# Kernel tuning notes

Hardware: AMD Instinct MI355X
Metric: run time of the kernel (lower is better)

## Reference

```python
import jax, jax.numpy as jnp
import numpy as np

B, HH, WW = 4, 112, 112
DIM, NH, WS, SHIFT = 384, 12, 7, 3
N = WS * WS
HD = DIM // NH
SCALE = HD ** -0.5
HID = DIM * 4
NW = (HH // WS) * (WW // WS)


def _ln(x, w, b):
    m = x.mean(-1, keepdims=True)
    v = ((x - m) ** 2).mean(-1, keepdims=True)
    return (x - m) / jnp.sqrt(v + 1e-5) * w + b


def _win_part(x):  # (B,H,W,C) -> (B*nW, N, C)
    x = x.reshape(B, HH // WS, WS, WW // WS, WS, DIM).transpose(0, 1, 3, 2, 4, 5)
    return x.reshape(-1, N, DIM)


def _win_rev(w):  # (B*nW, N, C) -> (B,H,W,C)
    x = w.reshape(B, HH // WS, WW // WS, WS, WS, DIM).transpose(0, 1, 3, 2, 4, 5)
    return x.reshape(B, HH, WW, DIM)


def _rel_index():
    c = np.arange(WS)
    coords = np.stack(np.meshgrid(c, c, indexing='ij')).reshape(2, -1)
    rel = (coords[:, :, None] - coords[:, None, :]).transpose(1, 2, 0).copy()
    rel[:, :, 0] += WS - 1
    rel[:, :, 1] += WS - 1
    rel[:, :, 0] *= 2 * WS - 1
    return rel.sum(-1)  # (N, N)


def _attn_mask():
    img = np.zeros((HH, WW))
    cnt = 0
    for hs in (slice(0, -WS), slice(-WS, -SHIFT), slice(-SHIFT, None)):
        for ws_ in (slice(0, -WS), slice(-WS, -SHIFT), slice(-SHIFT, None)):
            img[hs, ws_] = cnt
            cnt += 1
    mw = img.reshape(HH // WS, WS, WW // WS, WS).transpose(0, 2, 1, 3).reshape(-1, N)
    am = mw[:, None, :] - mw[:, :, None]
    return np.where(am != 0, -100.0, 0.0).astype(np.float32)  # (nW, N, N)


def setup_inputs():
    key = jax.random.key(0)
    ks = iter(jax.random.split(key, 32))
    rn = lambda shape, s=0.02: jax.random.normal(next(ks), shape, jnp.float32) * s
    return {
        'branch_1': jax.random.normal(next(ks), (B, HH * WW, DIM), jnp.float32),
        'branch_2': jax.random.normal(next(ks), (B, HH * WW, DIM), jnp.float32),
        'mask_matrix': jnp.asarray(_attn_mask()),
        'rpi': jnp.asarray(_rel_index(), jnp.int32),
        'n1w1': jnp.ones((DIM,)), 'n1b1': jnp.zeros((DIM,)),
        'n1w2': jnp.ones((DIM,)), 'n1b2': jnp.zeros((DIM,)),
        'qw1': rn((3 * DIM, DIM)), 'qb1': jnp.zeros((3 * DIM,)),
        'qw2': rn((3 * DIM, DIM)), 'qb2': jnp.zeros((3 * DIM,)),
        'rpb1': rn(((2 * WS - 1) ** 2, NH)), 'rpb2': rn(((2 * WS - 1) ** 2, NH)),
        'pw1': rn((DIM, DIM)), 'pb1': jnp.zeros((DIM,)),
        'pw2': rn((DIM, DIM)), 'pb2': jnp.zeros((DIM,)),
        'n2w1': jnp.ones((DIM,)), 'n2b1': jnp.zeros((DIM,)),
        'n2w2': jnp.ones((DIM,)), 'n2b2': jnp.zeros((DIM,)),
        'm1fc1w': rn((HID, DIM)), 'm1fc1b': jnp.zeros((HID,)),
        'm1fc2w': rn((DIM, HID)), 'm1fc2b': jnp.zeros((DIM,)),
        'm2fc1w': rn((HID, DIM)), 'm2fc1b': jnp.zeros((HID,)),
        'm2fc2w': rn((DIM, HID)), 'm2fc2b': jnp.zeros((DIM,)),
    }


def _cross_attn(x1, x2, mask, rpi, qw1, qb1, qw2, qb2, rpb1, rpb2, pw1, pb1, pw2, pb2):
    Bw = x1.shape[0]

    def qkv(x, w, b):
        t = (x @ w.T + b).reshape(Bw, N, 3, NH, HD).transpose(2, 0, 3, 1, 4)
        return t[0], t[1], t[2]

    q1, k1, v1 = qkv(x1, qw1, qb1)
    q2, k2, v2 = qkv(x2, qw2, qb2)
    a1 = (q2 * SCALE) @ jnp.swapaxes(k1, -2, -1)  # (Bw, NH, N, N)
    a2 = (q1 * SCALE) @ jnp.swapaxes(k2, -2, -1)
    b1 = rpb1[rpi].transpose(2, 0, 1)  # (NH, N, N)
    b2 = rpb2[rpi].transpose(2, 0, 1)
    a1 = a1 + b1[None]
    a2 = a2 + b2[None]
    nW = mask.shape[0]
    a1 = (a1.reshape(Bw // nW, nW, NH, N, N) + mask[None, :, None]).reshape(Bw, NH, N, N)
    a2 = (a2.reshape(Bw // nW, nW, NH, N, N) + mask[None, :, None]).reshape(Bw, NH, N, N)
    a1 = jax.nn.softmax(a1, axis=-1)
    a2 = jax.nn.softmax(a2, axis=-1)
    o1 = (a1 @ v1).transpose(0, 2, 1, 3).reshape(Bw, N, DIM) @ pw1.T + pb1
    o2 = (a2 @ v2).transpose(0, 2, 1, 3).reshape(Bw, N, DIM) @ pw2.T + pb2
    del o2
    return o1, o1  # faithful to original: it returns [branch_1, branch_1]


def _mlp(x, w1, b1, w2, b2):
    return jax.nn.gelu(x @ w1.T + b1, approximate=False) @ w2.T + b2


def reference(branch_1, branch_2, mask_matrix, rpi, n1w1, n1b1, n1w2, n1b2,
              qw1, qb1, qw2, qb2, rpb1, rpb2, pw1, pb1, pw2, pb2,
              n2w1, n2b1, n2w2, n2b2,
              m1fc1w, m1fc1b, m1fc2w, m1fc2b, m2fc1w, m2fc1b, m2fc2w, m2fc2b):
    s1, s2 = branch_1, branch_2
    x1 = _ln(branch_1, n1w1, n1b1).reshape(B, HH, WW, DIM)
    x2 = _ln(branch_2, n1w2, n1b2).reshape(B, HH, WW, DIM)
    # cyclic shift (shift_size > 0; H,W divisible by window_size so no padding)
    x1 = jnp.roll(x1, (-SHIFT, -SHIFT), (1, 2))
    x2 = jnp.roll(x2, (-SHIFT, -SHIFT), (1, 2))
    w1, w2 = _win_part(x1), _win_part(x2)
    o1, o2 = _cross_attn(w1, w2, mask_matrix, rpi, qw1, qb1, qw2, qb2,
                         rpb1, rpb2, pw1, pb1, pw2, pb2)
    y1 = jnp.roll(_win_rev(o1), (SHIFT, SHIFT), (1, 2)).reshape(B, HH * WW, DIM)
    y2 = jnp.roll(_win_rev(o2), (SHIFT, SHIFT), (1, 2)).reshape(B, HH * WW, DIM)
    b1 = s1 + y1
    b2 = s2 + y2
    out1 = b1 + _mlp(_ln(b1, n2w1, n2b1), m1fc1w, m1fc1b, m1fc2w, m1fc2b)
    out2 = b2 + _mlp(_ln(b2, n2w2, n2b2), m2fc1w, m2fc1b, m2fc2w, m2fc2b)
    return out1, out2
```

## Files before the change

### kernel.cpp

```cpp
#include <hip/hip_runtime.h>
#include <math.h>

#define DEV __device__ __forceinline__

typedef __attribute__((ext_vector_type(8))) unsigned short u16x8;
typedef __attribute__((ext_vector_type(8))) __bf16 bf16x8;
typedef __attribute__((ext_vector_type(4))) float f32x4;

static constexpr int TOK = 50176;
static constexpr int DIMC = 384;
static constexpr float QSCALE = 0.17677669529663687f;

DEV unsigned short f2bf(float f) {
  union { float f; unsigned u; } v; v.f = f;
  unsigned r = v.u + 0x7fffu + ((v.u >> 16) & 1u);
  return (unsigned short)(r >> 16);
}

DEV f32x4 mfma16(bf16x8 a, bf16x8 b, f32x4 c) {
  return __builtin_amdgcn_mfma_f32_16x16x32_bf16(a, b, c, 0, 0, 0);
}

DEV void gload_lds16(const void* g, void* lds) {
  __builtin_amdgcn_global_load_lds(
      (const __attribute__((address_space(1))) void*)g,
      (__attribute__((address_space(3))) void*)lds, 16, 0, 0);
}

__global__ __launch_bounds__(256) void w2bf_kern(const float* __restrict__ in,
                                                 unsigned short* __restrict__ out, int n) {
  int i = blockIdx.x * 256 + threadIdx.x;
  if (i < n) out[i] = f2bf(in[i]);
}

template<bool WINDOW>
__global__ __launch_bounds__(256) void ln_kern(const float* __restrict__ in,
                                               const float* __restrict__ gw,
                                               const float* __restrict__ gb,
                                               unsigned short* __restrict__ out) {
  const int row = blockIdx.x * 4 + (threadIdx.x >> 6);
  const int l = threadIdx.x & 63;
  int src = row;
  if (WINDOW) {
    const int wq = row / 49, nn = row - wq * 49;
    const int bb = wq >> 8, wi = wq & 255;
    int hh = (wi >> 4) * 7 + nn / 7 + 3;        if (hh >= 112) hh -= 112;
    int cc = (wi & 15) * 7 + (nn - (nn / 7) * 7) + 3; if (cc >= 112) cc -= 112;
    src = bb * 12544 + hh * 112 + cc;
  }
  const float* x = in + (size_t)src * DIMC;
  float v[6]; float s = 0.f, s2 = 0.f;
#pragma unroll
  for (int j = 0; j < 6; ++j) { float t = x[l + 64 * j]; v[j] = t; s += t; s2 += t * t; }
#pragma unroll
  for (int d = 1; d < 64; d <<= 1) { s += __shfl_xor(s, d); s2 += __shfl_xor(s2, d); }
  const float mean = s * (1.f / 384.f);
  const float var = s2 * (1.f / 384.f) - mean * mean;
  const float rs = rsqrtf(var + 1e-5f);
#pragma unroll
  for (int j = 0; j < 6; ++j) {
    int c = l + 64 * j;
    out[(size_t)row * DIMC + c] = f2bf((v[j] - mean) * rs * gw[c] + gb[c]);
  }
}

enum { E_BF16 = 0, E_BF16_SCALE = 1, E_SCATTER = 2, E_GELU = 3, E_RESOUT = 4 };

template<int EPI>
__global__ __launch_bounds__(256) void gemm_bt(
    const unsigned short* __restrict__ A, const unsigned short* __restrict__ W,
    const float* __restrict__ bias, int K, int N,
    unsigned short* __restrict__ outb,
    float* __restrict__ outf1, float* __restrict__ outf2,
    const float* __restrict__ res1, const float* __restrict__ res2) {
  __shared__ __align__(16) unsigned short sA[128 * 32];
  __shared__ __align__(16) unsigned short sB[128 * 32];
  const int t = threadIdx.x;
  const int wv = t >> 6, l = t & 63;
  const int wm = (wv >> 1) * 64, wn = (wv & 1) * 64;
  const int m0 = blockIdx.x * 128, n0 = blockIdx.y * 128;
  const int srow = t >> 2, scol = (t & 3) * 8;

  f32x4 acc[4][4];
  const f32x4 fzero = {0.f, 0.f, 0.f, 0.f};
#pragma unroll
  for (int i = 0; i < 4; ++i)
#pragma unroll
    for (int j = 0; j < 4; ++j) acc[i][j] = fzero;

  const unsigned short* gA = A + (size_t)(m0 + srow) * K + scol;
  const unsigned short* gB = W + (size_t)(n0 + srow) * K + scol;

  for (int kt = 0; kt < K; kt += 32) {
    __syncthreads();
#pragma unroll
    for (int it = 0; it < 2; ++it) {
      gload_lds16(gA + (size_t)it * 64 * K + kt, &sA[it * 2048 + wv * 512]);
      gload_lds16(gB + (size_t)it * 64 * K + kt, &sB[it * 2048 + wv * 512]);
    }
    __syncthreads();
    bf16x8 af[4], bff[4];
#pragma unroll
    for (int mt = 0; mt < 4; ++mt)
      af[mt] = *(const bf16x8*)&sA[(wm + mt * 16 + (l & 15)) * 32 + ((l >> 4) << 3)];
#pragma unroll
    for (int nt = 0; nt < 4; ++nt)
      bff[nt] = *(const bf16x8*)&sB[(wn + nt * 16 + (l & 15)) * 32 + ((l >> 4) << 3)];
#pragma unroll
    for (int mt = 0; mt < 4; ++mt)
#pragma unroll
      for (int nt = 0; nt < 4; ++nt) acc[mt][nt] = mfma16(af[mt], bff[nt], acc[mt][nt]);
  }

  const int g = l >> 4, col = l & 15;
#pragma unroll
  for (int mt = 0; mt < 4; ++mt) {
#pragma unroll
    for (int r = 0; r < 4; ++r) {
      const int m = m0 + wm + mt * 16 + g * 4 + r;
      size_t obase = 0;
      if constexpr (EPI == E_SCATTER) {
        int wq = m / 49, nn = m - wq * 49;
        int bb = wq >> 8, wi = wq & 255;
        int hh = (wi >> 4) * 7 + nn / 7 + 3;        if (hh >= 112) hh -= 112;
        int cc = (wi & 15) * 7 + (nn - (nn / 7) * 7) + 3; if (cc >= 112) cc -= 112;
        obase = ((size_t)bb * 12544 + hh * 112 + cc) * 384;
      }
#pragma unroll
      for (int nt = 0; nt < 4; ++nt) {
        const int j = n0 + wn + nt * 16 + col;
        float v = acc[mt][nt][r] + bias[j];
        if constexpr (EPI == E_BF16) {
          outb[(size_t)m * N + j] = f2bf(v);
        } else if constexpr (EPI == E_BF16_SCALE) {
          outb[(size_t)m * N + j] = f2bf(v * QSCALE);
        } else if constexpr (EPI == E_GELU) {
          outb[(size_t)m * N + j] = f2bf(0.5f * v * (1.f + erff(v * 0.70710678118654752f)));
        } else if constexpr (EPI == E_SCATTER) {
          outf1[obase + j] = res1[obase + j] + v;
          outf2[obase + j] = res2[obase + j] + v;
        } else {
          outf1[(size_t)m * N + j] = v + res1[(size_t)m * N + j];
        }
      }
    }
  }
}

__global__ __launch_bounds__(256) void attn_kern(
    const unsigned short* __restrict__ q2,
    const unsigned short* __restrict__ kv1,
    const int* __restrict__ rpi,
    const float* __restrict__ mask,
    const float* __restrict__ rpb,
    unsigned short* __restrict__ o) {
  const int w = blockIdx.x, h = blockIdx.y;
  __shared__ __align__(16) unsigned short sQ[64 * 32];
  __shared__ __align__(16) unsigned short sK[64 * 32];
  __shared__ __align__(16) unsigned short sVT[32 * 64];
  __shared__ __align__(16) unsigned short sP[64 * 64];
  const int t = threadIdx.x, wv = t >> 6, l = t & 63;
  const int r = t >> 2, c = (t & 3) * 8;
  const u16x8 z8 = {0, 0, 0, 0, 0, 0, 0, 0};
  if (r < 49) {
    *(u16x8*)&sQ[r * 32 + c] = *(const u16x8*)&q2[((size_t)w * 49 + r) * 384 + h * 32 + c];
    *(u16x8*)&sK[r * 32 + c] = *(const u16x8*)&kv1[((size_t)w * 49 + r) * 768 + h * 32 + c];
    u16x8 vv = *(const u16x8*)&kv1[((size_t)w * 49 + r) * 768 + 384 + h * 32 + c];
#pragma unroll
    for (int e = 0; e < 8; ++e) sVT[(c + e) * 64 + r] = vv[e];
  } else {
    *(u16x8*)&sQ[r * 32 + c] = z8;
    *(u16x8*)&sK[r * 32 + c] = z8;
#pragma unroll
    for (int e = 0; e < 8; ++e) sVT[(c + e) * 64 + r] = 0;
  }
  __syncthreads();

  const int g = l >> 4, col = l & 15;
  const f32x4 fzero = {0.f, 0.f, 0.f, 0.f};
  bf16x8 aq = *(const bf16x8*)&sQ[(wv * 16 + col) * 32 + g * 8];
  f32x4 s[4];
#pragma unroll
  for (int nt = 0; nt < 4; ++nt) {
    bf16x8 bk = *(const bf16x8*)&sK[(nt * 16 + col) * 32 + g * 8];
    s[nt] = mfma16(aq, bk, fzero);
  }

  const int wi = w & 255;
  float p[4][4];
#pragma unroll
  for (int rr = 0; rr < 4; ++rr) {
    const int i = wv * 16 + g * 4 + rr;
    float mx = -1e30f;
#pragma unroll
    for (int nt = 0; nt < 4; ++nt) {
      const int j = nt * 16 + col;
      float val = -1e9f;
      if (i < 49 && j < 49)
        val = s[nt][rr] + rpb[rpi[i * 49 + j] * 12 + h] + mask[((size_t)wi * 49 + i) * 49 + j];
      p[nt][rr] = val;
      mx = fmaxf(mx, val);
    }
#pragma unroll
    for (int d = 1; d < 16; d <<= 1) mx = fmaxf(mx, __shfl_xor(mx, d));
    float sm = 0.f;
#pragma unroll
    for (int nt = 0; nt < 4; ++nt) {
      const int j = nt * 16 + col;
      float e = (j < 49) ? __expf(p[nt][rr] - mx) : 0.f;
      p[nt][rr] = e; sm += e;
    }
#pragma unroll
    for (int d = 1; d < 16; d <<= 1) sm += __shfl_xor(sm, d);
    const float inv = 1.f / sm;
#pragma unroll
    for (int nt = 0; nt < 4; ++nt) p[nt][rr] *= inv;
  }
#pragma unroll
  for (int rr = 0; rr < 4; ++rr) {
    const int i = wv * 16 + g * 4 + rr;
#pragma unroll
    for (int nt = 0; nt < 4; ++nt) sP[i * 64 + nt * 16 + col] = f2bf(p[nt][rr]);
  }
  __syncthreads();

  f32x4 oa[2] = {fzero, fzero};
#pragma unroll
  for (int ks = 0; ks < 2; ++ks) {
    bf16x8 ap = *(const bf16x8*)&sP[(wv * 16 + col) * 64 + ks * 32 + g * 8];
#pragma unroll
    for (int n2 = 0; n2 < 2; ++n2) {
      bf16x8 bv = *(const bf16x8*)&sVT[(n2 * 16 + col) * 64 + ks * 32 + g * 8];
      oa[n2] = mfma16(ap, bv, oa[n2]);
    }
  }
#pragma unroll
  for (int rr = 0; rr < 4; ++rr) {
    const int i = wv * 16 + g * 4 + rr;
    if (i < 49) {
#pragma unroll
      for (int n2 = 0; n2 < 2; ++n2)
        o[((size_t)w * 49 + i) * 384 + h * 32 + n2 * 16 + col] = f2bf(oa[n2][rr]);
    }
  }
}

extern "C" void kernel_launch(void* const* d_in, const int* in_sizes, int n_in,
                              void* d_out, int out_size, void* d_ws, size_t ws_size,
                              hipStream_t stream) {
  (void)in_sizes; (void)n_in; (void)out_size; (void)ws_size;
  const float* s1   = (const float*)d_in[0];
  const float* s2   = (const float*)d_in[1];
  const float* mask = (const float*)d_in[2];
  const int*   rpi  = (const int*)d_in[3];
  const float* n1w1 = (const float*)d_in[4],  *n1b1 = (const float*)d_in[5];
  const float* n1w2 = (const float*)d_in[6],  *n1b2 = (const float*)d_in[7];
  const float* qw1  = (const float*)d_in[8],  *qb1  = (const float*)d_in[9];
  const float* qw2  = (const float*)d_in[10], *qb2  = (const float*)d_in[11];
  const float* rpb1 = (const float*)d_in[12];
  const float* pw1  = (const float*)d_in[14], *pb1  = (const float*)d_in[15];
  const float* n2w1 = (const float*)d_in[18], *n2b1 = (const float*)d_in[19];
  const float* n2w2 = (const float*)d_in[20], *n2b2 = (const float*)d_in[21];
  const float* m1fc1w = (const float*)d_in[22], *m1fc1b = (const float*)d_in[23];
  const float* m1fc2w = (const float*)d_in[24], *m1fc2b = (const float*)d_in[25];
  const float* m2fc1w = (const float*)d_in[26], *m2fc1b = (const float*)d_in[27];
  const float* m2fc2w = (const float*)d_in[28], *m2fc2b = (const float*)d_in[29];

  char* ws = (char*)d_ws;
  const size_t S1 = (size_t)TOK * DIMC * 2;
  unsigned short* x1w  = (unsigned short*)(ws);
  unsigned short* x2w  = (unsigned short*)(ws + S1);
  unsigned short* kv1  = (unsigned short*)(ws + 2 * S1);
  unsigned short* q2b  = (unsigned short*)(ws + 4 * S1);
  unsigned short* obuf = x1w;
  unsigned short* hbuf = x2w;
  unsigned short* xm   = x1w;
  char* wp = ws + 5 * S1;
  unsigned short* wq1b = (unsigned short*)(wp);
  unsigned short* wq2b = (unsigned short*)(wp + 589824);
  unsigned short* wp1b = (unsigned short*)(wp + 884736);
  unsigned short* wf11 = (unsigned short*)(wp + 1179648);
  unsigned short* wf12 = (unsigned short*)(wp + 2359296);
  unsigned short* wf21 = (unsigned short*)(wp + 3538944);
  unsigned short* wf22 = (unsigned short*)(wp + 4718592);

  float* outf = (float*)d_out;
  float* b1 = outf;
  float* b2 = outf + (size_t)19267584;

  w2bf_kern<<<(294912 + 255) / 256, 256, 0, stream>>>(qw1 + 384 * 384, wq1b, 294912);
  w2bf_kern<<<(147456 + 255) / 256, 256, 0, stream>>>(qw2, wq2b, 147456);
  w2bf_kern<<<(147456 + 255) / 256, 256, 0, stream>>>(pw1, wp1b, 147456);
  w2bf_kern<<<(589824 + 255) / 256, 256, 0, stream>>>(m1fc1w, wf11, 589824);
  w2bf_kern<<<(589824 + 255) / 256, 256, 0, stream>>>(m1fc2w, wf12, 589824);
  w2bf_kern<<<(589824 + 255) / 256, 256, 0, stream>>>(m2fc1w, wf21, 589824);
  w2bf_kern<<<(589824 + 255) / 256, 256, 0, stream>>>(m2fc2w, wf22, 589824);

  ln_kern<true><<<TOK / 4, 256, 0, stream>>>(s1, n1w1, n1b1, x1w);
  ln_kern<true><<<TOK / 4, 256, 0, stream>>>(s2, n1w2, n1b2, x2w);

  gemm_bt<E_BF16><<<dim3(392, 6), 256, 0, stream>>>(x1w, wq1b, qb1 + 384, 384, 768,
                                                    kv1, nullptr, nullptr, nullptr, nullptr);
  gemm_bt<E_BF16_SCALE><<<dim3(392, 3), 256, 0, stream>>>(x2w, wq2b, qb2, 384, 384,
                                                          q2b, nullptr, nullptr, nullptr, nullptr);
  attn_kern<<<dim3(1024, 12), 256, 0, stream>>>(q2b, kv1, rpi, mask, rpb1, obuf);

  gemm_bt<E_SCATTER><<<dim3(392, 3), 256, 0, stream>>>(obuf, wp1b, pb1, 384, 384,
                                                       nullptr, b1, b2, s1, s2);
  ln_kern<false><<<TOK / 4, 256, 0, stream>>>(b1, n2w1, n2b1, xm);
  gemm_bt<E_GELU><<<dim3(392, 12), 256, 0, stream>>>(xm, wf11, m1fc1b, 384, 1536,
                                                     hbuf, nullptr, nullptr, nullptr, nullptr);
  gemm_bt<E_RESOUT><<<dim3(392, 3), 256, 0, stream>>>(hbuf, wf12, m1fc2b, 1536, 384,
                                                      nullptr, b1, nullptr, b1, nullptr);
  ln_kern<false><<<TOK / 4, 256, 0, stream>>>(b2, n2w2, n2b2, xm);
  gemm_bt<E_GELU><<<dim3(392, 12), 256, 0, stream>>>(xm, wf21, m2fc1b, 384, 1536,
                                                     hbuf, nullptr, nullptr, nullptr, nullptr);
  gemm_bt<E_RESOUT><<<dim3(392, 3), 256, 0, stream>>>(hbuf, wf22, m2fc2b, 1536, 384,
                                                      nullptr, b2, nullptr, b2, nullptr);
}
```

Measured before the change: 925.5 us.

## Double-buffer GEMM LDS tiles with BK=64 and XOR-swizzled layout

The bf16 GEMM mainloop now prefetches the next 64-wide K tile into a second LDS buffer while MFMAs run on the current one. It uses a vmcnt wait plus a raw s_barrier in place of two __syncthreads per step. The K tile grows from 32 to 64, and an XOR swizzle of the column chunk by row removes LDS bank conflicts on fragment reads. The aim is to hide global-load latency and cut barrier overhead, at the cost of four times the LDS per block (64KB), which may lower occupancy.

```diff
diff --git a/kernel.cpp b/kernel.cpp
--- a/kernel.cpp
+++ b/kernel.cpp
@@ -73,13 +73,14 @@
     unsigned short* __restrict__ outb,
     float* __restrict__ outf1, float* __restrict__ outf2,
     const float* __restrict__ res1, const float* __restrict__ res2) {
-  __shared__ __align__(16) unsigned short sA[128 * 32];
-  __shared__ __align__(16) unsigned short sB[128 * 32];
+  __shared__ __align__(16) unsigned short sA[2][128 * 64];
+  __shared__ __align__(16) unsigned short sB[2][128 * 64];
   const int t = threadIdx.x;
   const int wv = t >> 6, l = t & 63;
   const int wm = (wv >> 1) * 64, wn = (wv & 1) * 64;
   const int m0 = blockIdx.x * 128, n0 = blockIdx.y * 128;
-  const int srow = t >> 2, scol = (t & 3) * 8;
+  const int srow = t >> 3;
+  const int scol = ((t & 7) ^ (srow & 7)) * 8;
 
   f32x4 acc[4][4];
   const f32x4 fzero = {0.f, 0.f, 0.f, 0.f};
@@ -90,29 +91,55 @@
 
   const unsigned short* gA = A + (size_t)(m0 + srow) * K + scol;
   const unsigned short* gB = W + (size_t)(n0 + srow) * K + scol;
-
-  for (int kt = 0; kt < K; kt += 32) {
-    __syncthreads();
-#pragma unroll
-    for (int it = 0; it < 2; ++it) {
-      gload_lds16(gA + (size_t)it * 64 * K + kt, &sA[it * 2048 + wv * 512]);
-      gload_lds16(gB + (size_t)it * 64 * K + kt, &sB[it * 2048 + wv * 512]);
-    }
-    __syncthreads();
-    bf16x8 af[4], bff[4];
-#pragma unroll
-    for (int mt = 0; mt < 4; ++mt)
-      af[mt] = *(const bf16x8*)&sA[(wm + mt * 16 + (l & 15)) * 32 + ((l >> 4) << 3)];
-#pragma unroll
-    for (int nt = 0; nt < 4; ++nt)
-      bff[nt] = *(const bf16x8*)&sB[(wn + nt * 16 + (l & 15)) * 32 + ((l >> 4) << 3)];
-#pragma unroll
-    for (int mt = 0; mt < 4; ++mt)
-#pragma unroll
-      for (int nt = 0; nt < 4; ++nt) acc[mt][nt] = mfma16(af[mt], bff[nt], acc[mt][nt]);
-  }
-
-  const int g = l >> 4, col = l & 15;
+  const int ldsW = wv * 512;
+
+  const int g = l >> 4, lr = l & 15;
+  const int swz = (lr & 7) << 4;
+
+  const int ntt = K >> 6;
+#pragma unroll
+  for (int it = 0; it < 4; ++it) {
+    gload_lds16(gA + (size_t)(it * 32) * K, &sA[0][it * 2048 + ldsW]);
+    gload_lds16(gB + (size_t)(it * 32) * K, &sB[0][it * 2048 + ldsW]);
+  }
+  for (int tt = 0; tt < ntt; ++tt) {
+    const int cur = tt & 1;
+    if (tt + 1 < ntt) {
+      const int kt = (tt + 1) << 6;
+#pragma unroll
+      for (int it = 0; it < 4; ++it) {
+        gload_lds16(gA + (size_t)(it * 32) * K + kt, &sA[cur ^ 1][it * 2048 + ldsW]);
+        gload_lds16(gB + (size_t)(it * 32) * K + kt, &sB[cur ^ 1][it * 2048 + ldsW]);
+      }
+      asm volatile("s_waitcnt vmcnt(8)" ::: "memory");
+    } else {
+      asm volatile("s_waitcnt vmcnt(0)" ::: "memory");
+    }
+    __builtin_amdgcn_s_barrier();
+    asm volatile("" ::: "memory");
+    const char* bA = (const char*)&sA[cur][0];
+    const char* bB = (const char*)&sB[cur][0];
+#pragma unroll
+    for (int ks = 0; ks < 2; ++ks) {
+      bf16x8 af[4], bff[4];
+      const int cb = (ks * 64 + g * 16) ^ swz;
+#pragma unroll
+      for (int mt = 0; mt < 4; ++mt)
+        af[mt] = *(const bf16x8*)(bA + (wm + mt * 16 + lr) * 128 + cb);
+#pragma unroll
+      for (int nt2 = 0; nt2 < 4; ++nt2)
+        bff[nt2] = *(const bf16x8*)(bB + (wn + nt2 * 16 + lr) * 128 + cb);
+#pragma unroll
+      for (int mt = 0; mt < 4; ++mt)
+#pragma unroll
+        for (int nt2 = 0; nt2 < 4; ++nt2)
+          acc[mt][nt2] = mfma16(af[mt], bff[nt2], acc[mt][nt2]);
+    }
+    asm volatile("" ::: "memory");
+    __builtin_amdgcn_s_barrier();
+  }
+
+  const int col = lr;
 #pragma unroll
   for (int mt = 0; mt < 4; ++mt) {
 #pragma unroll
@@ -127,9 +154,9 @@
         obase = ((size_t)bb * 12544 + hh * 112 + cc) * 384;
       }
 #pragma unroll
-      for (int nt = 0; nt < 4; ++nt) {
-        const int j = n0 + wn + nt * 16 + col;
-        float v = acc[mt][nt][r] + bias[j];
+      for (int nt2 = 0; nt2 < 4; ++nt2) {
+        const int j = n0 + wn + nt2 * 16 + col;
+        float v = acc[mt][nt2][r] + bias[j];
         if constexpr (EPI == E_BF16) {
           outb[(size_t)m * N + j] = f2bf(v);
         } else if constexpr (EPI == E_BF16_SCALE) {
```

New measurement: 877.3 us. 5.2% less time.
